# Kernel optimization log

Measured on AMD Instinct MI355X. Metric: run time of the kernel, lower is better.

Reference implementation:

```python
import jax, jax.numpy as jnp
import numpy as np
from jax import lax

B, T, D, H, W, K, E = 2, 16, 128, 64, 64, 3, 4


def setup_inputs() -> dict:
    key = jax.random.key(0)
    ks = jax.random.split(key, 20)

    def rn(k, shape, s):
        return (jax.random.normal(k, shape) * s).astype(jnp.float32)

    D2 = 2 * D
    inp = {
        "x_re": jax.random.normal(ks[0], (B, T, D, H, W), jnp.float32),
        "x_im": jax.random.normal(ks[1], (B, T, D, H, W), jnp.float32),
        # keep dt in [0.1, 1.0] (physical timestep, avoids sqrt(0) in noise term)
        "dt": (jax.random.uniform(ks[2], (B, T)) * 0.9 + 0.1).astype(jnp.float32),
        "ln_s_g": jnp.ones((D2,), jnp.float32),
        "ln_s_b": jnp.zeros((D2,), jnp.float32),
        "ln_t_g": jnp.ones((D2,), jnp.float32),
        "ln_t_b": jnp.zeros((D2,), jnp.float32),
        "conv_metric": (1.0 + 0.02 * jax.random.normal(ks[3], (D2, H, W))).astype(jnp.float32),
        "conv_w": rn(ks[4], (D2, D2, K, K), 1.0 / np.sqrt(D2 * K * K)),
        "conv_b": jnp.zeros((D2,), jnp.float32),
        "nu": rn(ks[5], (D,), 0.5),
        "theta": rn(ks[6], (D,), 1.0),
        "enc_re": rn(ks[7], (D, D), 1.0 / np.sqrt(D)),
        "enc_im": rn(ks[8], (D, D), 1.0 / np.sqrt(D)),
        "dec_re": rn(ks[9], (D, D), 1.0 / np.sqrt(D)),
        "dec_im": rn(ks[10], (D, D), 1.0 / np.sqrt(D)),
        "src_gain": rn(ks[11], (D,), 0.1),
        "w1_re": rn(ks[12], (D, E * D), 1.0 / np.sqrt(D)),
        "w1_im": rn(ks[13], (D, E * D), 1.0 / np.sqrt(D)),
        "b1_re": jnp.zeros((E * D,), jnp.float32),
        "b1_im": jnp.zeros((E * D,), jnp.float32),
        "w2_re": rn(ks[14], (E * D, D), 1.0 / np.sqrt(E * D)),
        "w2_im": rn(ks[15], (E * D, D), 1.0 / np.sqrt(E * D)),
        "b2_re": jnp.zeros((D,), jnp.float32),
        "b2_im": jnp.zeros((D,), jnp.float32),
    }
    return inp


def _ln(x, g, b):
    m = jnp.mean(x, -1, keepdims=True)
    v = jnp.var(x, -1, keepdims=True)
    return (x - m) * lax.rsqrt(v + 1e-5) * g + b


def _cnorm(z, g, b):
    # complex LayerNorm: LN over concat(real, imag) along last dim, then re-pack
    zn = _ln(jnp.concatenate([z.real, z.imag], -1), g, b)
    r, i = jnp.split(zn, 2, -1)
    return lax.complex(r, i)


def _forward(x_re, x_im, dt, ln_s_g, ln_s_b, ln_t_g, ln_t_b, conv_metric, conv_w, conv_b,
             nu, theta, enc_re, enc_im, dec_re, dec_im, src_gain,
             w1_re, w1_im, b1_re, b1_im, w2_re, w2_im, b2_re, b2_im):
    x = lax.complex(x_re, x_im)  # [B,T,D,H,W] complex64
    Bb, Tt, Dd, Hh, Ww = x.shape
    resid = x
    # ---- spatial branch: complex LN + metric-scaled (Riemannian) Clifford conv ----
    xs = jnp.transpose(x.reshape(Bb * Tt, Dd, Hh, Ww), (0, 2, 3, 1))  # [BT,H,W,D]
    xs = jnp.transpose(_cnorm(xs, ln_s_g, ln_s_b), (0, 3, 1, 2))      # [BT,D,H,W]
    xri = jnp.concatenate([xs.real, xs.imag], 1) * conv_metric[None]  # [BT,2D,H,W]
    pad = K // 2
    oc = lax.conv_general_dilated(xri, conv_w, (1, 1), ((pad, pad), (pad, pad)),
                                  dimension_numbers=("NCHW", "OIHW", "NCHW"))
    oc = oc + conv_b[None, :, None, None]
    r, i = jnp.split(oc, 2, 1)
    x = lax.complex(r, i).reshape(Bb, Tt, Dd, Hh, Ww) + resid
    resid = x
    # ---- temporal branch: eigen-encode, source law, ZOH forcing, parallel scan ----
    xt = jnp.transpose(x, (0, 3, 4, 1, 2)).reshape(Bb * Hh * Ww, Tt, Dd)  # [N,T,D]
    xt = _cnorm(xt, ln_t_g, ln_t_b)
    dte = jnp.broadcast_to(dt[:, None, None, :], (Bb, Hh, Ww, Tt)).reshape(Bb * Hh * Ww, Tt)
    lam = lax.complex(-jax.nn.softplus(nu), theta)                 # [D], Re<0 (stable)
    op_decay = jnp.exp(lam[None, None, :] * dte[:, :, None])       # [N,T,D] complex
    op_forcing = (op_decay - 1.0) / lam                            # zero-order hold
    xe = xt @ lax.complex(enc_re, enc_im)                          # eigenbasis encode
    src = lax.complex(jnp.tanh(xe.real), jnp.tanh(xe.imag)) * src_gain
    u = (xe + src) * op_forcing
    # stochastic term (fixed key -> deterministic reference)
    nk1, nk2 = jax.random.split(jax.random.key(42))
    amp = 0.01 * jnp.sqrt(dte)[:, :, None]
    u = u + lax.complex(amp * jax.random.normal(nk1, u.shape),
                        amp * jax.random.normal(nk2, u.shape))

    def comb(c1, c2):  # h_t = a_t * h_{t-1} + u_t
        a1, u1 = c1
        a2, u2 = c2
        return a1 * a2, a2 * u1 + u2

    _, h = lax.associative_scan(comb, (op_decay, u), axis=1)       # [N,T,D]
    xo = h @ lax.complex(dec_re, dec_im)                           # eigenbasis decode
    x_drift = jnp.transpose(xo.real.reshape(Bb, Hh, Ww, Tt, Dd), (0, 3, 4, 1, 2))
    x = x_drift + resid
    # ---- complex pointwise FFN ----
    z = jnp.transpose(x, (0, 1, 3, 4, 2))                          # [B,T,H,W,D]
    hdn = z @ lax.complex(w1_re, w1_im) + lax.complex(b1_re, b1_im)
    act = lax.complex(jax.nn.gelu(hdn.real), jax.nn.gelu(hdn.imag))
    delta = act @ lax.complex(w2_re, w2_im) + lax.complex(b2_re, b2_im)
    x = x + jnp.transpose(delta, (0, 1, 4, 2, 3))
    return jnp.stack([x.real, x.imag], -1)  # [B,T,D,H,W,2] float32


def reference(x_re, x_im, dt, ln_s_g, ln_s_b, ln_t_g, ln_t_b, conv_metric, conv_w, conv_b,
              nu, theta, enc_re, enc_im, dec_re, dec_im, src_gain,
              w1_re, w1_im, b1_re, b1_im, w2_re, w2_im, b2_re, b2_im):
    return _forward(x_re, x_im, dt, ln_s_g, ln_s_b, ln_t_g, ln_t_b, conv_metric, conv_w,
                    conv_b, nu, theta, enc_re, enc_im, dec_re, dec_im, src_gain,
                    w1_re, w1_im, b1_re, b1_im, w2_re, w2_im, b2_re, b2_im)
```

## Files before the change

kernel.cpp:

```cpp
#include <hip/hip_runtime.h>
#include <hip/hip_bf16.h>
#include <stdint.h>

#define B_   2
#define T_   16
#define D_   128
#define D2_  256
#define H_   64
#define W_   64
#define HW_  4096
#define BT_  32
#define N_   8192
#define ND_  1048576
#define PLANE_ 16777216
#define WT_FLOATS 589824

typedef short bf16x8 __attribute__((ext_vector_type(8)));
typedef float f32x4 __attribute__((ext_vector_type(4)));
typedef unsigned int uint;
typedef unsigned short ushort;


__device__ __forceinline__ float softplus_f(float x) {
  return fmaxf(x, 0.0f) + log1pf(expf(-fabsf(x)));
}

__device__ __forceinline__ float gelu_fast(float x) {
  const float Ac = 2.3022082963f;
  const float Bc = 0.1029437f;
  float t = x * x;
  float z = x * fmaf(Bc, t, Ac);
  float e = __builtin_amdgcn_exp2f(z);
  float r = __builtin_amdgcn_rcpf(e + 1.0f);
  return fmaf(-x, r, x);
}

__device__ __forceinline__ float tanh_fast(float x) {
  float e = __builtin_amdgcn_exp2f(x * 2.8853900818f);
  float r = __builtin_amdgcn_rcpf(e + 1.0f);
  return fmaf(-2.0f, r, 1.0f);
}

__device__ __forceinline__ ushort f2bf(float f) {
  uint u = __float_as_uint(f);
  uint r = (u + 0x7fffu + ((u >> 16) & 1u)) >> 16;
  return (ushort)r;
}

__device__ __forceinline__ uint cvt_pk(float a, float b) {
  __hip_bfloat162 h = __float22bfloat162_rn(make_float2(a, b));
  return *reinterpret_cast<uint*>(&h);
}


__global__ __launch_bounds__(256) void k_spatial_ln(
    const float* __restrict__ x_re, const float* __restrict__ x_im,
    const float* __restrict__ g, const float* __restrict__ bb,
    const float* __restrict__ metric, ushort* __restrict__ xri) {
  __shared__ float vals[256][64];
  __shared__ float red1[4][64];
  __shared__ float red2[4][64];
  __shared__ float mean_s[64];
  __shared__ float rstd_s[64];
  const int blk = blockIdx.x;
  const int bt = blk >> 6;
  const int h = blk & 63;
  const int tid = threadIdx.x;
  const int w = tid & 63, q = tid >> 6;

  const float* src = (q < 2) ? x_re : x_im;
  float s1 = 0.f, s2 = 0.f;
  #pragma unroll 4
  for (int i = 0; i < 64; ++i) {
    const int c = q * 64 + i;
    const int d = c & 127;
    float v = src[((size_t)bt * D_ + d) * HW_ + h * W_ + w];
    vals[c][w] = v;
    s1 += v; s2 += v * v;
  }
  red1[q][w] = s1; red2[q][w] = s2;
  __syncthreads();
  if (tid < 64) {
    float m = red1[0][tid] + red1[1][tid] + red1[2][tid] + red1[3][tid];
    float ss = red2[0][tid] + red2[1][tid] + red2[2][tid] + red2[3][tid];
    m *= (1.f / 256.f);
    float var = ss * (1.f / 256.f) - m * m;
    mean_s[tid] = m;
    rstd_s[tid] = rsqrtf(var + 1e-5f);
  }
  __syncthreads();
  const float m = mean_s[w], rs = rstd_s[w];
  const size_t ubase = (((size_t)bt * 64 + h) * 32 + q * 8) * 512 + w * 8;
  #pragma unroll
  for (int j = 0; j < 8; ++j) {
    uint4 u;
    #pragma unroll
    for (int e2 = 0; e2 < 4; ++e2) {
      const int c0 = q * 64 + j * 8 + e2 * 2;
      float v0 = (vals[c0][w] - m) * rs * g[c0] + bb[c0];
      v0 *= metric[(size_t)c0 * HW_ + h * W_ + w];
      float v1 = (vals[c0 + 1][w] - m) * rs * g[c0 + 1] + bb[c0 + 1];
      v1 *= metric[(size_t)(c0 + 1) * HW_ + h * W_ + w];
      ((uint*)&u)[e2] = cvt_pk(v0, v1);
    }
    *(uint4*)&xri[ubase + (size_t)j * 512] = u;
  }
}


__global__ __launch_bounds__(256) void k_prep_conv(
    const float* __restrict__ wg, ushort* __restrict__ cwswz) {
  const int t = blockIdx.x * 256 + threadIdx.x;
  if (t >= 73728) return;
  const int lane = t & 63;
  const int nt = (t >> 6) & 15;
  const int ks = (t >> 10) & 7;
  const int kk = t >> 13;
  const int co = nt * 16 + (lane & 15);
  const int ci0 = ks * 32 + (lane >> 4) * 8;
  ushort v[8];
  #pragma unroll
  for (int e = 0; e < 8; ++e)
    v[e] = f2bf(wg[((size_t)co * 256 + ci0 + e) * 9 + kk]);
  uint4 u;
  u.x = (uint)v[0] | ((uint)v[1] << 16);
  u.y = (uint)v[2] | ((uint)v[3] << 16);
  u.z = (uint)v[4] | ((uint)v[5] << 16);
  u.w = (uint)v[6] | ((uint)v[7] << 16);
  ((uint4*)cwswz)[t] = u;
}


__global__ __launch_bounds__(512, 4) void k_conv_mfma(
    const ushort* __restrict__ xri, const ushort* __restrict__ cwswz,
    const float* __restrict__ bias,
    const float* __restrict__ x_re, const float* __restrict__ x_im,
    uint* __restrict__ x2p) {
  __shared__ ushort xb[33792];
  const int tid = threadIdx.x;
  const int wave = tid >> 6, lane = tid & 63;
  const int lrow = lane & 15, lgrp = lane >> 4;
  const int blk = blockIdx.x;
  const int bt = blk >> 5;
  const int h0 = (blk & 31) * 2;
  const int cw = wave & 3;
  const int sg = wave >> 2;

  f32x4 acc[4][4];
  #pragma unroll
  for (int j = 0; j < 4; ++j)
    #pragma unroll
    for (int i = 0; i < 4; ++i) acc[j][i] = (f32x4)0.f;

  for (int half = 0; half < 2; ++half) {
    __syncthreads();
    if (tid < 128) {
      const int j = tid >> 5;
      const int u = (tid >> 1) & 15;
      const int wz = (tid & 1) * 65;
      uint4 z = {0u, 0u, 0u, 0u};
      *(uint4*)&xb[((j * 16 + u) * 66 + wz) * 8] = z;
    }
    #pragma unroll
    for (int i = 0; i < 8; ++i) {
      const int idx = i * 512 + tid;
      const int w = idx & 63;
      const int u = (idx >> 6) & 15;
      const int j = idx >> 10;
      const int hh = h0 + j - 1;
      uint4 v = {0u, 0u, 0u, 0u};
      if (hh >= 0 && hh < 64)
        v = *(const uint4*)&xri[(((size_t)bt * 64 + hh) * 32 + half * 16 + u) * 512
                                + w * 8];
      *(uint4*)&xb[((j * 16 + u) * 66 + 1 + w) * 8] = v;
    }
    __syncthreads();

    for (int kh = 0; kh < 3; ++kh) {
      for (int kw = 0; kw < 3; ++kw) {
        const int kk = kh * 3 + kw;
        #pragma unroll
        for (int ks = 0; ks < 4; ++ks) {
          bf16x8 bfr[4];
          #pragma unroll
          for (int i = 0; i < 4; ++i)
            bfr[i] = *(const bf16x8*)&xb[(((sg + kh) * 16 + ks * 4 + lgrp) * 66
                                          + i * 16 + lrow + kw) * 8];
          const int fbase = ((kk * 8 + half * 4 + ks) * 16 + cw * 4) * 64 + lane;
          #pragma unroll
          for (int j = 0; j < 4; ++j) {
            const bf16x8 afr = ((const bf16x8*)cwswz)[fbase + j * 64];
            #pragma unroll
            for (int i = 0; i < 4; ++i)
              acc[j][i] = __builtin_amdgcn_mfma_f32_16x16x32_bf16(
                  afr, bfr[i], acc[j][i], 0, 0, 0);
          }
        }
      }
    }
  }

  __syncthreads();
  if (cw >= 2) {
    #pragma unroll
    for (int j = 0; j < 4; ++j) {
      #pragma unroll
      for (int jj = 0; jj < 4; ++jj) {
        const int co = (cw * 4 + j) * 16 + lgrp * 4 + jj;
        const int d = co - 128;
        const float bv = bias[co];
        const size_t rowoff = ((size_t)bt * D_ + d) * HW_ + (h0 + sg) * W_;
        #pragma unroll
        for (int i = 0; i < 4; ++i) {
          const int w = i * 16 + lrow;
          const float imv = acc[j][i][jj] + bv + x_im[rowoff + w];
          xb[(sg * 64 + w) * 132 + d] = f2bf(imv);
        }
      }
    }
  }
  __syncthreads();
  if (cw < 2) {
    #pragma unroll
    for (int j = 0; j < 4; ++j) {
      #pragma unroll
      for (int jj = 0; jj < 4; ++jj) {
        const int d = (cw * 4 + j) * 16 + lgrp * 4 + jj;
        const float bv = bias[d];
        const size_t rowoff = ((size_t)bt * D_ + d) * HW_ + (h0 + sg) * W_;
        #pragma unroll
        for (int i = 0; i < 4; ++i) {
          const int w = i * 16 + lrow;
          const float rev = acc[j][i][jj] + bv + x_re[rowoff + w];
          const uint im16 = xb[(sg * 64 + w) * 132 + d];
          x2p[rowoff + w] = (uint)f2bf(rev) | (im16 << 16);
        }
      }
    }
  }
}


__global__ __launch_bounds__(256) void k_prep_decay(
    const float* __restrict__ dt, const float* __restrict__ nu,
    const float* __restrict__ theta, float4* __restrict__ decay) {
  const int idx = blockIdx.x * 256 + threadIdx.x;
  const int d = idx & 127;
  const int bt = idx >> 7;
  const float dtv = dt[bt];
  const float lr = -softplus_f(nu[d]);
  const float li = theta[d];
  float s, c;
  sincosf(li * dtv, &s, &c);
  const float er = expf(lr * dtv);
  const float ar = er * c, ai = er * s;
  const float den = lr * lr + li * li;
  const float nr = ar - 1.f, ni = ai;
  float4 v;
  v.x = ar; v.y = ai;
  v.z = (nr * lr + ni * li) / den;
  v.w = (ni * lr - nr * li) / den;
  decay[idx] = v;
}


__global__ __launch_bounds__(256) void k_prep_enc(
    const float* __restrict__ enc_re, const float* __restrict__ enc_im,
    const float* __restrict__ g, ushort* __restrict__ encswz) {
  const int t = blockIdx.x * 256 + threadIdx.x;
  const int lane = t & 63;
  const int ks = (t >> 6) & 7;
  const int ntile = t >> 9;
  const int n = ntile * 16 + (lane & 15);
  const int k0 = ks * 32 + (lane >> 4) * 8;
  ushort v[8];
  #pragma unroll
  for (int e = 0; e < 8; ++e) {
    const int kp = k0 + e;
    const int k = (kp >> 1) | ((kp & 1) << 7);
    float val;
    if (k < 128) {
      val = (n < 128) ? enc_re[k * 128 + n] : enc_im[k * 128 + (n - 128)];
    } else {
      const int kk = k - 128;
      val = (n < 128) ? -enc_im[kk * 128 + n] : enc_re[kk * 128 + (n - 128)];
    }
    v[e] = f2bf(val * g[k]);
  }
  uint4 u;
  u.x = (uint)v[0] | ((uint)v[1] << 16);
  u.y = (uint)v[2] | ((uint)v[3] << 16);
  u.z = (uint)v[4] | ((uint)v[5] << 16);
  u.w = (uint)v[6] | ((uint)v[7] << 16);
  ((uint4*)encswz)[t] = u;
}

__global__ __launch_bounds__(256) void k_prep_encvec(
    const float* __restrict__ enc_re, const float* __restrict__ enc_im,
    const float* __restrict__ g, const float* __restrict__ bb,
    float* __restrict__ evec, float* __restrict__ cvec) {
  const int n = threadIdx.x;
  float se = 0.f, sc = 0.f;
  for (int k = 0; k < 256; ++k) {
    float ep;
    if (k < 128) {
      ep = (n < 128) ? enc_re[k * 128 + n] : enc_im[k * 128 + (n - 128)];
    } else {
      const int kk = k - 128;
      ep = (n < 128) ? -enc_im[kk * 128 + n] : enc_re[kk * 128 + (n - 128)];
    }
    se = fmaf(g[k], ep, se);
    sc = fmaf(bb[k], ep, sc);
  }
  evec[n] = se;
  cvec[n] = sc;
}

__global__ __launch_bounds__(256) void k_prep_dec(
    const float* __restrict__ dec_re, const float* __restrict__ dec_im,
    ushort* __restrict__ decswz) {
  const int t = blockIdx.x * 256 + threadIdx.x;
  const int lane = t & 63;
  const int ks = (t >> 6) & 7;
  const int ntile = t >> 9;
  const int n = ntile * 16 + (lane & 15);
  const int k0 = ks * 32 + (lane >> 4) * 8;
  ushort v[8];
  #pragma unroll
  for (int e = 0; e < 8; ++e) {
    const int kp = k0 + e;
    const int k = (kp >> 1) | ((kp & 1) << 7);
    float val = (k < 128) ? dec_re[k * 128 + n] : -dec_im[(k - 128) * 128 + n];
    v[e] = f2bf(val);
  }
  uint4 u;
  u.x = (uint)v[0] | ((uint)v[1] << 16);
  u.y = (uint)v[2] | ((uint)v[3] << 16);
  u.z = (uint)v[4] | ((uint)v[5] << 16);
  u.w = (uint)v[6] | ((uint)v[7] << 16);
  ((uint4*)decswz)[t] = u;
}


__global__ __launch_bounds__(256, 2) void k_temporal_mfma(
    const uint* __restrict__ x2p,
    const ushort* __restrict__ encswz,
    const float* __restrict__ evec, const float* __restrict__ cvec,
    const float4* __restrict__ decay,
    const float* __restrict__ src_gain,
    uint* __restrict__ u32) {
  __shared__ ushort xlds[64][256];
  __shared__ float red1[4][64], red2[4][64];
  __shared__ float mean_s[64], rstd_s[64];
  __shared__ float fre_s[128], fim_s[128], gain_s[128];
  const int tid = threadIdx.x;
  const int wave = tid >> 6, lane = tid & 63;
  const int lrow = lane & 15, lgrp = lane >> 4;
  const int blk = blockIdx.x;
  const int h = blk & 63;
  const int t = (blk >> 6) & 15;
  const int b = blk >> 10;
  const int bt = b * T_ + t;

  float s1 = 0.f, s2 = 0.f;
  #pragma unroll
  for (int i = 0; i < 8; ++i) {
    const int q = i * 4 + wave;
    const uint* src = &x2p[((size_t)bt * D_ + q * 4) * HW_ + h * W_ + lane];
    uint4 u;
    u.x = src[0];
    u.y = src[HW_];
    u.z = src[2 * HW_];
    u.w = src[3 * HW_];
    *(uint4*)&xlds[lane][(q ^ (lane & 7)) << 3] = u;
    #pragma unroll
    for (int e = 0; e < 4; ++e) {
      const uint v = ((const uint*)&u)[e];
      const float re = __uint_as_float(v << 16);
      const float im = __uint_as_float(v & 0xffff0000u);
      s1 += re + im;
      s2 += re * re + im * im;
    }
  }
  red1[wave][lane] = s1;
  red2[wave][lane] = s2;
  __syncthreads();
  if (tid < 64) {
    float m = red1[0][tid] + red1[1][tid] + red1[2][tid] + red1[3][tid];
    float ss = red2[0][tid] + red2[1][tid] + red2[2][tid] + red2[3][tid];
    m *= (1.f / 256.f);
    float var = ss * (1.f / 256.f) - m * m;
    mean_s[tid] = m;
    rstd_s[tid] = rsqrtf(var + 1e-5f);
  }
  if (tid < 128) {
    const float4 dc = decay[bt * 128 + tid];
    fre_s[tid] = dc.z;
    fim_s[tid] = dc.w;
    gain_s[tid] = src_gain[tid];
  }
  __syncthreads();

  f32x4 acc[4][4];
  #pragma unroll
  for (int ntl = 0; ntl < 4; ++ntl)
    #pragma unroll
    for (int st = 0; st < 4; ++st) acc[ntl][st] = (f32x4)0.f;

  const int swz = lrow & 7;
  const int ntb[4] = {wave * 2, wave * 2 + 1, wave * 2 + 8, wave * 2 + 9};
  #pragma unroll
  for (int ks = 0; ks < 8; ++ks) {
    bf16x8 bfr[4];
    #pragma unroll
    for (int st = 0; st < 4; ++st)
      bfr[st] = *(const bf16x8*)&xlds[st * 16 + lrow][(((ks * 4 + lgrp) ^ swz)) << 3];
    #pragma unroll
    for (int ntl = 0; ntl < 4; ++ntl) {
      const bf16x8 afr = ((const bf16x8*)encswz)[(ntb[ntl] * 8 + ks) * 64 + lane];
      #pragma unroll
      for (int st = 0; st < 4; ++st)
        acc[ntl][st] = __builtin_amdgcn_mfma_f32_16x16x32_bf16(
            afr, bfr[st], acc[ntl][st], 0, 0, 0);
    }
  }

  const int nbase = (b * 64 + h) * 64;
  #pragma unroll
  for (int ntl = 0; ntl < 2; ++ntl) {
    const int d0 = ntb[ntl] * 16 + lgrp * 4;
    #pragma unroll
    for (int st = 0; st < 4; ++st) {
      const int site = st * 16 + lrow;
      const float m = mean_s[site], rs = rstd_s[site];
      #pragma unroll
      for (int j = 0; j < 4; ++j) {
        const int d = d0 + j;
        const float xer = rs * acc[ntl][st][j] - rs * m * evec[d] + cvec[d];
        const float xei = rs * acc[ntl + 2][st][j] - rs * m * evec[d + 128] + cvec[d + 128];
        const float sr = tanh_fast(xer) * gain_s[d];
        const float si = tanh_fast(xei) * gain_s[d];
        const float vr = xer + sr, vi = xei + si;
        const float ur = vr * fre_s[d] - vi * fim_s[d];
        const float ui = vr * fim_s[d] + vi * fre_s[d];
        u32[(size_t)t * ND_ + (size_t)d * N_ + nbase + site] = cvt_pk(ur, ui);
      }
    }
  }
}


__global__ __launch_bounds__(256) void k_scan(
    uint* __restrict__ u32, const float4* __restrict__ decay) {
  const int idx = blockIdx.x * 256 + threadIdx.x;
  const int n = idx & 8191;
  const int d = idx >> 13;
  const int b = n >> 12;
  float hr = 0.f, hi = 0.f;
  #pragma unroll
  for (int t = 0; t < 16; ++t) {
    const float4 dc = decay[(b * 16 + t) * 128 + d];
    const size_t off = (size_t)t * ND_ + idx;
    const uint v = u32[off];
    const float ur = __uint_as_float(v << 16);
    const float ui = __uint_as_float(v & 0xffff0000u);
    const float nr = fmaf(dc.x, hr, fmaf(-dc.y, hi, ur));
    const float ni = fmaf(dc.x, hi, fmaf(dc.y, hr, ui));
    hr = nr; hi = ni;
    u32[off] = cvt_pk(hr, hi);
  }
}


__global__ __launch_bounds__(256) void k_prep_b1(
    const float* __restrict__ w1_re, const float* __restrict__ w1_im,
    ushort* __restrict__ b1swz) {
  const int t = blockIdx.x * 256 + threadIdx.x;
  const int lane = t & 63;
  const int ks = (t >> 6) & 7;
  const int ntile = t >> 9;
  const int n = ntile * 16 + (lane & 15);
  const int k0 = ks * 32 + (lane >> 4) * 8;
  ushort v[8];
  #pragma unroll
  for (int e = 0; e < 8; ++e) {
    const int kp = k0 + e;
    const int k = (kp >> 1) | ((kp & 1) << 7);
    float val;
    if (k < 128) {
      val = (n < 512) ? w1_re[k * 512 + n] : w1_im[k * 512 + (n - 512)];
    } else {
      const int kk = k - 128;
      val = (n < 512) ? -w1_im[kk * 512 + n] : w1_re[kk * 512 + (n - 512)];
    }
    v[e] = f2bf(val);
  }
  uint4 u;
  u.x = (uint)v[0] | ((uint)v[1] << 16);
  u.y = (uint)v[2] | ((uint)v[3] << 16);
  u.z = (uint)v[4] | ((uint)v[5] << 16);
  u.w = (uint)v[6] | ((uint)v[7] << 16);
  ((uint4*)b1swz)[t] = u;
}

__global__ __launch_bounds__(256) void k_prep_b2(
    const float* __restrict__ w2_re, const float* __restrict__ w2_im,
    ushort* __restrict__ b2swz) {
  const int t = blockIdx.x * 256 + threadIdx.x;
  const int lane = t & 63;
  const int kc = (t >> 6) & 31;
  const int rowtile = t >> 11;
  const int n2 = rowtile * 16 + (lane & 15);
  const int k0 = kc * 32 + (lane >> 4) * 8;
  ushort v[8];
  #pragma unroll
  for (int e = 0; e < 8; ++e) {
    const int k = k0 + e;
    float val;
    if (k < 512) {
      val = (n2 < 128) ? w2_re[k * 128 + n2] : w2_im[k * 128 + (n2 - 128)];
    } else {
      const int kk = k - 512;
      val = (n2 < 128) ? -w2_im[kk * 128 + n2] : w2_re[kk * 128 + (n2 - 128)];
    }
    v[e] = f2bf(val);
  }
  uint4 u;
  u.x = (uint)v[0] | ((uint)v[1] << 16);
  u.y = (uint)v[2] | ((uint)v[3] << 16);
  u.z = (uint)v[4] | ((uint)v[5] << 16);
  u.w = (uint)v[6] | ((uint)v[7] << 16);
  ((uint4*)b2swz)[t] = u;
}


__global__ __launch_bounds__(256, 2) void k_ffn_mfma(
    const uint* __restrict__ x2p, const uint* __restrict__ h32,
    const ushort* __restrict__ decswz,
    const ushort* __restrict__ b1swz, const ushort* __restrict__ b2swz,
    const float* __restrict__ b1_re, const float* __restrict__ b1_im,
    const float* __restrict__ b2_re, const float* __restrict__ b2_im,
    float* __restrict__ out) {
  __shared__ ushort xlds[64][256];
  __shared__ ushort actlds[2][64][136];
  const int tid = threadIdx.x;
  const int wave = tid >> 6, lane = tid & 63;
  const int lrow = lane & 15, lgrp = lane >> 4;
  const int blk = blockIdx.x;
  const int bt = blk >> 6;
  const int hrow = blk & 63;
  const int hw0 = hrow * 64;
  const int b = bt >> 4, t = bt & 15;
  const int nbase = (b * 64 + hrow) * 64;
  const bf16x8* b1f = (const bf16x8*)b1swz;
  const bf16x8* b2f = (const bf16x8*)b2swz;
  const bf16x8* dcf = (const bf16x8*)decswz;
  ushort* hbuf = &actlds[0][0][0];

  #pragma unroll
  for (int i = 0; i < 8; ++i) {
    const int q = i * 4 + wave;
    const uint* src = &x2p[((size_t)bt * D_ + q * 4) * HW_ + hw0 + lane];
    uint4 u;
    u.x = src[0]; u.y = src[HW_]; u.z = src[2 * HW_]; u.w = src[3 * HW_];
    *(uint4*)&xlds[lane][(q ^ (lane & 7)) << 3] = u;
  }
  #pragma unroll
  for (int i = 0; i < 8; ++i) {
    const int q = i * 4 + wave;
    const size_t o = (size_t)t * ND_ + (size_t)(q * 4) * N_ + nbase + lane;
    uint4 u;
    u.x = h32[o]; u.y = h32[o + N_]; u.z = h32[o + 2 * N_]; u.w = h32[o + 3 * N_];
    *(uint4*)&hbuf[lane * 264 + ((q ^ (lane & 7)) << 3)] = u;
  }

  bf16x8 a1[2][8];
  #pragma unroll
  for (int ntl = 0; ntl < 2; ++ntl)
    #pragma unroll
    for (int ks = 0; ks < 8; ++ks)
      a1[ntl][ks] = b1f[((wave * 2 + ntl) * 8 + ks) * 64 + lane];
  bf16x8 a2[4][2];
  #pragma unroll
  for (int rt = 0; rt < 4; ++rt)
    #pragma unroll
    for (int k2 = 0; k2 < 2; ++k2)
      a2[rt][k2] = b2f[((wave * 4 + rt) * 32 + k2) * 64 + lane];

  __syncthreads();
  const int swz = lrow & 7;

  {
    f32x4 dr[2][4];
    #pragma unroll
    for (int ntl = 0; ntl < 2; ++ntl)
      #pragma unroll
      for (int st = 0; st < 4; ++st) dr[ntl][st] = (f32x4)0.f;
    #pragma unroll
    for (int ks = 0; ks < 8; ++ks) {
      bf16x8 bfr[4];
      #pragma unroll
      for (int st = 0; st < 4; ++st)
        bfr[st] = *(const bf16x8*)&hbuf[(st * 16 + lrow) * 264
                                        + (((ks * 4 + lgrp) ^ swz) << 3)];
      #pragma unroll
      for (int ntl = 0; ntl < 2; ++ntl) {
        const bf16x8 afr = dcf[((wave * 2 + ntl) * 8 + ks) * 64 + lane];
        #pragma unroll
        for (int st = 0; st < 4; ++st)
          dr[ntl][st] = __builtin_amdgcn_mfma_f32_16x16x32_bf16(
              afr, bfr[st], dr[ntl][st], 0, 0, 0);
      }
    }
    #pragma unroll
    for (int ntl = 0; ntl < 2; ++ntl) {
      #pragma unroll
      for (int st = 0; st < 4; ++st) {
        const int site = st * 16 + lrow;
        #pragma unroll
        for (int j = 0; j < 4; ++j) {
          const int d = (wave * 2 + ntl) * 16 + lgrp * 4 + j;
          ushort* p = &xlds[site][(((d >> 2) ^ (site & 7)) << 3) + (d & 3) * 2];
          const uint v = *(uint*)p;
          const float re = __uint_as_float(v << 16) + dr[ntl][st][j];
          *(uint*)p = (v & 0xffff0000u) | (uint)f2bf(re);
        }
      }
    }
  }
  __syncthreads();

  f32x4 dacc[4][4];
  #pragma unroll
  for (int rt = 0; rt < 4; ++rt)
    #pragma unroll
    for (int st = 0; st < 4; ++st) dacc[rt][st] = (f32x4)0.f;

  for (int chunk = 0; chunk < 8; ++chunk) {
    const int nc = (chunk + 1) & 7;

    f32x4 hacc[2][4];
    #pragma unroll
    for (int ntl = 0; ntl < 2; ++ntl)
      #pragma unroll
      for (int st = 0; st < 4; ++st) hacc[ntl][st] = (f32x4)0.f;

    #pragma unroll
    for (int ks = 0; ks < 8; ++ks) {
      bf16x8 bfr[4];
      #pragma unroll
      for (int st = 0; st < 4; ++st)
        bfr[st] = *(const bf16x8*)&xlds[st * 16 + lrow][(((ks * 4 + lgrp) ^ swz)) << 3];
      #pragma unroll
      for (int ntl = 0; ntl < 2; ++ntl)
        #pragma unroll
        for (int st = 0; st < 4; ++st)
          hacc[ntl][st] = __builtin_amdgcn_mfma_f32_16x16x32_bf16(
              a1[ntl][ks], bfr[st], hacc[ntl][st], 0, 0, 0);
    }

    #pragma unroll
    for (int ntl = 0; ntl < 2; ++ntl)
      #pragma unroll
      for (int ks = 0; ks < 8; ++ks)
        a1[ntl][ks] = b1f[((nc * 8 + wave * 2 + ntl) * 8 + ks) * 64 + lane];

    uint* act32 = (uint*)&actlds[chunk & 1][0][0];
    #pragma unroll
    for (int ntl = 0; ntl < 2; ++ntl) {
      const int nlocal0 = (wave * 2 + ntl) * 16 + lgrp * 4;
      const int ng0 = chunk * 128 + nlocal0;
      #pragma unroll
      for (int st = 0; st < 4; ++st) {
        float gv[4];
        #pragma unroll
        for (int j = 0; j < 4; ++j) {
          const int ng = ng0 + j;
          const float bias = (ng < 512) ? b1_re[ng] : b1_im[ng - 512];
          gv[j] = gelu_fast(hacc[ntl][st][j] + bias);
        }
        const int site = st * 16 + lrow;
        act32[site * 68 + (nlocal0 >> 1)] = cvt_pk(gv[0], gv[1]);
        act32[site * 68 + (nlocal0 >> 1) + 1] = cvt_pk(gv[2], gv[3]);
      }
    }

    bf16x8 a2b[4][2];
    #pragma unroll
    for (int rt = 0; rt < 4; ++rt)
      #pragma unroll
      for (int k2 = 0; k2 < 2; ++k2)
        a2b[rt][k2] = b2f[((wave * 4 + rt) * 32 + chunk * 4 + 2 + k2) * 64 + lane];

    __syncthreads();

    const ushort* actb = &actlds[chunk & 1][0][0];
    #pragma unroll
    for (int ks2 = 0; ks2 < 2; ++ks2) {
      bf16x8 bfr[4];
      #pragma unroll
      for (int st = 0; st < 4; ++st)
        bfr[st] = *(const bf16x8*)&actb[(st * 16 + lrow) * 136 + ks2 * 32 + lgrp * 8];
      #pragma unroll
      for (int rt = 0; rt < 4; ++rt)
        #pragma unroll
        for (int st = 0; st < 4; ++st)
          dacc[rt][st] = __builtin_amdgcn_mfma_f32_16x16x32_bf16(
              a2[rt][ks2], bfr[st], dacc[rt][st], 0, 0, 0);
    }
    #pragma unroll
    for (int ks2 = 0; ks2 < 2; ++ks2) {
      bf16x8 bfr[4];
      #pragma unroll
      for (int st = 0; st < 4; ++st)
        bfr[st] = *(const bf16x8*)&actb[(st * 16 + lrow) * 136 + (ks2 + 2) * 32 + lgrp * 8];
      #pragma unroll
      for (int rt = 0; rt < 4; ++rt)
        #pragma unroll
        for (int st = 0; st < 4; ++st)
          dacc[rt][st] = __builtin_amdgcn_mfma_f32_16x16x32_bf16(
              a2b[rt][ks2], bfr[st], dacc[rt][st], 0, 0, 0);
    }

    #pragma unroll
    for (int rt = 0; rt < 4; ++rt)
      #pragma unroll
      for (int k2 = 0; k2 < 2; ++k2)
        a2[rt][k2] = b2f[((wave * 4 + rt) * 32 + nc * 4 + k2) * 64 + lane];
  }

  #pragma unroll
  for (int rt = 0; rt < 4; ++rt) {
    #pragma unroll
    for (int j = 0; j < 4; ++j) {
      const int n2 = (wave * 4 + rt) * 16 + lgrp * 4 + j;
      const int d = n2 & 127;
      const int c = n2 >> 7;
      const float bias2 = c ? b2_im[d] : b2_re[d];
      #pragma unroll
      for (int st = 0; st < 4; ++st) {
        const int site = st * 16 + lrow;
        const uint pr = *(const uint*)&xlds[site][(((d >> 2) ^ (site & 7)) << 3)
                                                  + (d & 3) * 2];
        const float rv = c ? __uint_as_float(pr & 0xffff0000u)
                           : __uint_as_float(pr << 16);
        const size_t idx = (size_t)(bt * D_ + d) * HW_ + hw0 + site;
        out[idx * 2 + c] = rv + dacc[rt][st][j] + bias2;
      }
    }
  }
}


extern "C" void kernel_launch(void* const* d_in, const int* in_sizes, int n_in,
                              void* d_out, int out_size, void* d_ws, size_t ws_size,
                              hipStream_t stream) {
  const float* x_re   = (const float*)d_in[0];
  const float* x_im   = (const float*)d_in[1];
  const float* dt     = (const float*)d_in[2];
  const float* ln_s_g = (const float*)d_in[3];
  const float* ln_s_b = (const float*)d_in[4];
  const float* ln_t_g = (const float*)d_in[5];
  const float* ln_t_b = (const float*)d_in[6];
  const float* metric = (const float*)d_in[7];
  const float* conv_w = (const float*)d_in[8];
  const float* conv_b = (const float*)d_in[9];
  const float* nu     = (const float*)d_in[10];
  const float* theta  = (const float*)d_in[11];
  const float* enc_re = (const float*)d_in[12];
  const float* enc_im = (const float*)d_in[13];
  const float* dec_re = (const float*)d_in[14];
  const float* dec_im = (const float*)d_in[15];
  const float* src_g  = (const float*)d_in[16];
  const float* w1_re  = (const float*)d_in[17];
  const float* w1_im  = (const float*)d_in[18];
  const float* b1_re  = (const float*)d_in[19];
  const float* b1_im  = (const float*)d_in[20];
  const float* w2_re  = (const float*)d_in[21];
  const float* w2_im  = (const float*)d_in[22];
  const float* b2_re  = (const float*)d_in[23];
  const float* b2_im  = (const float*)d_in[24];
  float* out = (float*)d_out;
  float* ws = (float*)d_ws;

  float* wt   = ws;
  float* bufA = ws + WT_FLOATS;
  ushort* wt16  = (ushort*)wt;
  ushort* cwswz = wt16;
  ushort* b1swz = wt16;
  ushort* b2swz = wt16 + 262144;
  ushort* encswz = wt16 + 524288;
  ushort* decswz = wt16 + 589824;
  float*  evec   = (float*)(wt16 + 622592);
  float*  cvec   = evec + 256;
  float4* decay  = (float4*)(cvec + 256);
  ushort* xri_bf = (ushort*)bufA;

  const size_t needA = ((size_t)WT_FLOATS + 2 * (size_t)PLANE_) * 4 + (1u << 20);
  const bool planA = ws_size >= needA;
  uint *u32p, *x2p;
  float* ffn_out;
  if (planA) {
    u32p = (uint*)bufA;
    x2p  = (uint*)bufA + PLANE_;
    ffn_out = out;
  } else {
    u32p = (uint*)out;
    x2p  = (uint*)out + PLANE_;
    ffn_out = bufA;
  }

  k_prep_conv<<<288, 256, 0, stream>>>(conv_w, cwswz);
  k_prep_decay<<<16, 256, 0, stream>>>(dt, nu, theta, decay);
  k_spatial_ln<<<BT_ * H_, 256, 0, stream>>>(x_re, x_im, ln_s_g, ln_s_b, metric, xri_bf);
  k_conv_mfma<<<BT_ * 32, 512, 0, stream>>>(xri_bf, cwswz, conv_b, x_re, x_im, x2p);
  k_prep_b1<<<128, 256, 0, stream>>>(w1_re, w1_im, b1swz);
  k_prep_b2<<<128, 256, 0, stream>>>(w2_re, w2_im, b2swz);
  k_prep_enc<<<32, 256, 0, stream>>>(enc_re, enc_im, ln_t_g, encswz);
  k_prep_encvec<<<1, 256, 0, stream>>>(enc_re, enc_im, ln_t_g, ln_t_b, evec, cvec);
  k_prep_dec<<<16, 256, 0, stream>>>(dec_re, dec_im, decswz);
  k_temporal_mfma<<<B_ * T_ * H_, 256, 0, stream>>>(x2p, encswz, evec, cvec,
                                                    decay, src_g, u32p);
  k_scan<<<ND_ / 256, 256, 0, stream>>>(u32p, decay);
  k_ffn_mfma<<<BT_ * H_, 256, 0, stream>>>(x2p, u32p, decswz, b1swz, b2swz,
                                           b1_re, b1_im, b2_re, b2_im, ffn_out);
  if (!planA) {
    hipMemcpyAsync(d_out, ffn_out, (size_t)2 * PLANE_ * sizeof(float),
                   hipMemcpyDeviceToDevice, stream);
  }
}
```

Before: 664.8 us.

## Permute conv weight tiles so each wave owns real+imag channels, shrink LDS staging

The weight swizzle is reordered so each wave's four output tiles hold two real-channel tiles and the matching two imaginary-channel tiles. The epilogue can then pack real and imaginary results directly from registers, with no LDS round-trip or extra barriers. The input staging is split into four quarters of 64 channels instead of two halves, halving shared memory, and the launch bound is raised to target 8 blocks per CU. The cost is twice as many load/sync phases per block and possible register pressure under the tighter occupancy hint.

```diff
diff --git a/kernel.cpp b/kernel.cpp
--- a/kernel.cpp
+++ b/kernel.cpp
@@ -116,7 +116,9 @@
   const int nt = (t >> 6) & 15;
   const int ks = (t >> 10) & 7;
   const int kk = t >> 13;
-  const int co = nt * 16 + (lane & 15);
+  const int cwv = nt >> 2, jjv = nt & 3;
+  const int co_tile = (jjv < 2) ? (2 * cwv + jjv) : (8 + 2 * cwv + (jjv - 2));
+  const int co = co_tile * 16 + (lane & 15);
   const int ci0 = ks * 32 + (lane >> 4) * 8;
   ushort v[8];
   #pragma unroll
@@ -131,12 +133,12 @@
 }
 
 
-__global__ __launch_bounds__(512, 4) void k_conv_mfma(
+__global__ __launch_bounds__(512, 8) void k_conv_mfma(
     const ushort* __restrict__ xri, const ushort* __restrict__ cwswz,
     const float* __restrict__ bias,
     const float* __restrict__ x_re, const float* __restrict__ x_im,
     uint* __restrict__ x2p) {
-  __shared__ ushort xb[33792];
+  __shared__ ushort xb[16896];
   const int tid = threadIdx.x;
   const int wave = tid >> 6, lane = tid & 63;
   const int lrow = lane & 15, lgrp = lane >> 4;
@@ -152,27 +154,27 @@
     #pragma unroll
     for (int i = 0; i < 4; ++i) acc[j][i] = (f32x4)0.f;
 
-  for (int half = 0; half < 2; ++half) {
+  for (int quarter = 0; quarter < 4; ++quarter) {
     __syncthreads();
-    if (tid < 128) {
-      const int j = tid >> 5;
-      const int u = (tid >> 1) & 15;
+    if (tid < 64) {
+      const int j = tid >> 4;
+      const int u = (tid >> 1) & 7;
       const int wz = (tid & 1) * 65;
       uint4 z = {0u, 0u, 0u, 0u};
-      *(uint4*)&xb[((j * 16 + u) * 66 + wz) * 8] = z;
-    }
-    #pragma unroll
-    for (int i = 0; i < 8; ++i) {
+      *(uint4*)&xb[((j * 8 + u) * 66 + wz) * 8] = z;
+    }
+    #pragma unroll
+    for (int i = 0; i < 4; ++i) {
       const int idx = i * 512 + tid;
       const int w = idx & 63;
-      const int u = (idx >> 6) & 15;
-      const int j = idx >> 10;
+      const int u = (idx >> 6) & 7;
+      const int j = idx >> 9;
       const int hh = h0 + j - 1;
       uint4 v = {0u, 0u, 0u, 0u};
       if (hh >= 0 && hh < 64)
-        v = *(const uint4*)&xri[(((size_t)bt * 64 + hh) * 32 + half * 16 + u) * 512
+        v = *(const uint4*)&xri[(((size_t)bt * 64 + hh) * 32 + quarter * 8 + u) * 512
                                 + w * 8];
-      *(uint4*)&xb[((j * 16 + u) * 66 + 1 + w) * 8] = v;
+      *(uint4*)&xb[((j * 8 + u) * 66 + 1 + w) * 8] = v;
     }
     __syncthreads();
 
@@ -180,13 +182,13 @@
       for (int kw = 0; kw < 3; ++kw) {
         const int kk = kh * 3 + kw;
         #pragma unroll
-        for (int ks = 0; ks < 4; ++ks) {
+        for (int ks = 0; ks < 2; ++ks) {
           bf16x8 bfr[4];
           #pragma unroll
           for (int i = 0; i < 4; ++i)
-            bfr[i] = *(const bf16x8*)&xb[(((sg + kh) * 16 + ks * 4 + lgrp) * 66
+            bfr[i] = *(const bf16x8*)&xb[(((sg + kh) * 8 + ks * 4 + lgrp) * 66
                                           + i * 16 + lrow + kw) * 8];
-          const int fbase = ((kk * 8 + half * 4 + ks) * 16 + cw * 4) * 64 + lane;
+          const int fbase = ((kk * 8 + quarter * 2 + ks) * 16 + cw * 4) * 64 + lane;
           #pragma unroll
           for (int j = 0; j < 4; ++j) {
             const bf16x8 afr = ((const bf16x8*)cwswz)[fbase + j * 64];
@@ -200,41 +202,20 @@
     }
   }
 
-  __syncthreads();
-  if (cw >= 2) {
-    #pragma unroll
-    for (int j = 0; j < 4; ++j) {
-      #pragma unroll
-      for (int jj = 0; jj < 4; ++jj) {
-        const int co = (cw * 4 + j) * 16 + lgrp * 4 + jj;
-        const int d = co - 128;
-        const float bv = bias[co];
-        const size_t rowoff = ((size_t)bt * D_ + d) * HW_ + (h0 + sg) * W_;
-        #pragma unroll
-        for (int i = 0; i < 4; ++i) {
-          const int w = i * 16 + lrow;
-          const float imv = acc[j][i][jj] + bv + x_im[rowoff + w];
-          xb[(sg * 64 + w) * 132 + d] = f2bf(imv);
-        }
-      }
-    }
-  }
-  __syncthreads();
-  if (cw < 2) {
-    #pragma unroll
-    for (int j = 0; j < 4; ++j) {
-      #pragma unroll
-      for (int jj = 0; jj < 4; ++jj) {
-        const int d = (cw * 4 + j) * 16 + lgrp * 4 + jj;
-        const float bv = bias[d];
-        const size_t rowoff = ((size_t)bt * D_ + d) * HW_ + (h0 + sg) * W_;
-        #pragma unroll
-        for (int i = 0; i < 4; ++i) {
-          const int w = i * 16 + lrow;
-          const float rev = acc[j][i][jj] + bv + x_re[rowoff + w];
-          const uint im16 = xb[(sg * 64 + w) * 132 + d];
-          x2p[rowoff + w] = (uint)f2bf(rev) | (im16 << 16);
-        }
+  #pragma unroll
+  for (int j = 0; j < 2; ++j) {
+    #pragma unroll
+    for (int jj = 0; jj < 4; ++jj) {
+      const int d = (2 * cw + j) * 16 + lgrp * 4 + jj;
+      const float bvr = bias[d];
+      const float bvi = bias[d + 128];
+      const size_t rowoff = ((size_t)bt * D_ + d) * HW_ + (h0 + sg) * W_;
+      #pragma unroll
+      for (int i = 0; i < 4; ++i) {
+        const int w = i * 16 + lrow;
+        const float re = acc[j][i][jj] + bvr + x_re[rowoff + w];
+        const float im = acc[j + 2][i][jj] + bvi + x_im[rowoff + w];
+        x2p[rowoff + w] = cvt_pk(re, im);
       }
     }
   }
```

New measurement: 1.997 ms. 3x slower.
